# Optimization experiments

Measured on AMD Instinct MI355X. Metric: run time of the kernel, lower is better.

The kernel has to match this reference:

```python
import jax, jax.numpy as jnp
import numpy as np
import math

# Config (matches init_kwargs)
H = 16        # n_heads
DH = 64       # n_dim_head
L = 8         # n_layers
D = 1024      # n_dim
FF = 4096     # n_dim_ffn
NNB = 1       # n_non_bias_tokens
B, T = 2, 1024
EPS = 1e-5


def _slopes(n):
    start = 2.0 ** (-2.0 ** (-(math.log2(n) - 3)))
    return -np.array([start * start ** i for i in range(n)], dtype=np.float32)


def _alibi(seq_len):
    cl = seq_len - NNB
    pos = np.arange(cl)
    rel = np.abs(pos[None, :] - pos[:, None]).astype(np.float32)  # [cl, cl]
    bias = _slopes(H)[:, None, None] * rel                         # [H, cl, cl]
    bias = np.pad(bias, ((0, 0), (0, NNB), (0, NNB)))              # [H, T, T]
    return jnp.asarray(bias)[None]                                  # [1, H, T, T]


def _ln(x, g):
    mu = jnp.mean(x, -1, keepdims=True)
    var = jnp.mean(jnp.square(x - mu), -1, keepdims=True)
    return (x - mu) * jax.lax.rsqrt(var + EPS) * g


def setup_inputs() -> dict:
    key = jax.random.key(0)
    ks = jax.random.split(key, 12)
    std = 0.02
    return {
        "x": jax.random.normal(ks[0], (B, T, D), jnp.float32),
        "attn_w": jax.random.normal(ks[1], (L, 3 * H * DH, D), jnp.float32) * std,
        "attn_out_w": jax.random.normal(ks[2], (L, D, H * DH), jnp.float32) * std,
        "mlp_ln_g": jnp.ones((L, D), jnp.float32),
        "mlp_in_w": jax.random.normal(ks[3], (L, FF, D), jnp.float32) * std,
        "mlp_in_b": jnp.zeros((L, FF), jnp.float32),
        "mlp_out_w": jax.random.normal(ks[4], (L, D, FF), jnp.float32) * std,
        "mlp_out_b": jnp.zeros((L, D), jnp.float32),
        "skip_w": jax.random.normal(ks[5], (L // 2, D, 2 * D), jnp.float32) * std,
        "skip_b": jnp.zeros((L // 2, D), jnp.float32),
        "out_ln_g": jnp.ones((D,), jnp.float32),
    }


def _block(x, alibi, aw, aow, mg, miw, mib, mow, mob):
    b, t, _ = x.shape
    # NOTE: original code computes attention_ln(x) but feeds raw x to the QKV
    # projection (LN output discarded) -- replicated faithfully here.
    qkv = jnp.einsum('btd,ed->bte', x, aw)                 # [B,T,3*H*DH]
    q, k, v = jnp.split(qkv, 3, axis=-1)
    def heads(z):
        return z.reshape(b, t, H, DH).transpose(0, 2, 1, 3)  # [B,H,T,DH]
    q, k, v = heads(q), heads(k), heads(v)
    scores = jnp.einsum('bhqd,bhkd->bhqk', q, k) / math.sqrt(DH) + alibi
    p = jax.nn.softmax(scores, axis=-1)
    o = jnp.einsum('bhqk,bhkd->bhqd', p, v)
    o = o.transpose(0, 2, 1, 3).reshape(b, t, H * DH)
    x = x + jnp.einsum('bte,de->btd', o, aow)
    h = _ln(x, mg)
    h = jax.nn.gelu(jnp.einsum('btd,fd->btf', h, miw) + mib, approximate=False)
    x = x + jnp.einsum('btf,df->btd', h, mow) + mob
    return x


def reference(x, attn_w, attn_out_w, mlp_ln_g, mlp_in_w, mlp_in_b,
              mlp_out_w, mlp_out_b, skip_w, skip_b, out_ln_g):
    _, t, _ = x.shape
    alibi = _alibi(t)
    half = L // 2
    connections = []
    for i in range(L):
        if L - half < i:
            s = connections.pop() * (2.0 ** -0.5)
            xc = jnp.concatenate([x, s], axis=-1)
            j = i - half
            x = jnp.einsum('bte,de->btd', xc, skip_w[j]) + skip_b[j]
        x = _block(x, alibi, attn_w[i], attn_out_w[i], mlp_ln_g[i],
                   mlp_in_w[i], mlp_in_b[i], mlp_out_w[i], mlp_out_b[i])
        if i <= half:
            connections.append(x)
    return _ln(x, out_ln_g)
```

## Files before the change

### kernel.cpp

```cpp
#include <hip/hip_runtime.h>
#include <hip/hip_bf16.h>
#include <math.h>

typedef unsigned short us;
typedef short bf16x8 __attribute__((ext_vector_type(8)));
typedef float f32x4 __attribute__((ext_vector_type(4)));
typedef unsigned short usx4 __attribute__((ext_vector_type(4)));

#define NT   2048
#define DDIM 1024
#define FF   4096
#define TT   1024
#define NH   16
#define CL   1023

__device__ __forceinline__ us f2bf(float f) {
  unsigned u = __float_as_uint(f);
  return (us)((u + 0x7FFFu + ((u >> 16) & 1u)) >> 16);
}

__device__ __forceinline__ void gld_lds16(const us* g, us* l) {
  __builtin_amdgcn_global_load_lds(
      (const __attribute__((address_space(1))) unsigned int*)(g),
      (__attribute__((address_space(3))) unsigned int*)(l), 16, 0, 0);
}

__device__ __forceinline__ void cast_seg(const float* s, us* d, int n4, int tid, int stride) {
  if (n4 <= 0) return;
  for (int i = tid; i < n4; i += stride) {
    float4 v = ((const float4*)s)[i];
    usx4 o; o.x = f2bf(v.x); o.y = f2bf(v.y); o.z = f2bf(v.z); o.w = f2bf(v.w);
    ((usx4*)d)[i] = o;
  }
}

__global__ void cast5_kernel(const float* s0, us* d0, int n0,
                             const float* s1, us* d1, int n1,
                             const float* s2, us* d2, int n2,
                             const float* s3, us* d3, int n3,
                             const float* s4, us* d4, int n4) {
  int tid = blockIdx.x * blockDim.x + threadIdx.x;
  int stride = gridDim.x * blockDim.x;
  cast_seg(s0, d0, n0, tid, stride);
  cast_seg(s1, d1, n1, tid, stride);
  cast_seg(s2, d2, n2, tid, stride);
  cast_seg(s3, d3, n3, tid, stride);
  cast_seg(s4, d4, n4, tid, stride);
}

__global__ void cast1_kernel(const float* s, us* d, int n4) {
  int tid = blockIdx.x * blockDim.x + threadIdx.x;
  int stride = gridDim.x * blockDim.x;
  cast_seg(s, d, n4, tid, stride);
}

template<int SET>
__global__ void bias_rows_kernel(float* __restrict__ x, const float* __restrict__ bias) {
  int i = blockIdx.x * blockDim.x + threadIdx.x;
  float4 b = ((const float4*)bias)[i & 255];
  if (SET) {
    ((float4*)x)[i] = b;
  } else {
    float4 v = ((float4*)x)[i];
    v.x += b.x; v.y += b.y; v.z += b.z; v.w += b.w;
    ((float4*)x)[i] = v;
  }
}

template<int MODE>
__global__ __launch_bounds__(256)
void gemm4(const us* __restrict__ A, const us* __restrict__ W,
           const float* __restrict__ bias, float* outf, us* outb,
           us* __restrict__ Qb, us* __restrict__ Kb, us* __restrict__ Vt,
           int M, int N, int K, int kchunk)
{
  __shared__ us As[64 * 32];
  __shared__ us Ws[128 * 32];
  const int tid = threadIdx.x;
  const int m0 = blockIdx.y * 64, n0 = blockIdx.x * 128;
  const int wave = tid >> 6, lane = tid & 63;
  const int wm = (wave & 1) * 32, wn = (wave >> 1) * 64;
  const int frow = lane & 15, fk = (lane >> 4) * 8;
  const int kbeg = blockIdx.z * kchunk, kend = kbeg + kchunk;
  const int ar = tid >> 2, ac = (tid & 3) * 8;
  const int wr1 = (256 + tid) >> 2;
  f32x4 acc[2][4] = {};
  for (int k0 = kbeg; k0 < kend; k0 += 32) {
    gld_lds16(A + (size_t)(m0 + ar) * K + k0 + ac, As + wave * 512);
    gld_lds16(W + (size_t)(n0 + ar) * K + k0 + ac, Ws + wave * 512);
    gld_lds16(W + (size_t)(n0 + wr1) * K + k0 + ac, Ws + 2048 + wave * 512);
    __syncthreads();
    bf16x8 afr[2], wfr[4];
    #pragma unroll
    for (int i = 0; i < 2; ++i) afr[i] = *(const bf16x8*)(As + (wm + i * 16 + frow) * 32 + fk);
    #pragma unroll
    for (int j = 0; j < 4; ++j) wfr[j] = *(const bf16x8*)(Ws + (wn + j * 16 + frow) * 32 + fk);
    #pragma unroll
    for (int i = 0; i < 2; ++i)
      #pragma unroll
      for (int j = 0; j < 4; ++j)
        acc[i][j] = __builtin_amdgcn_mfma_f32_16x16x32_bf16(afr[i], wfr[j], acc[i][j], 0, 0, 0);
    __syncthreads();
  }
  const int col = lane & 15, rq = (lane >> 4) * 4;
  #pragma unroll
  for (int i = 0; i < 2; ++i) {
    const int gmq = m0 + wm + i * 16 + rq;
    #pragma unroll
    for (int j = 0; j < 4; ++j) {
      const int gn = n0 + wn + j * 16 + col;
      if (MODE == 5) {
        const int t = gmq & (TT - 1), b = gmq >> 10;
        if (gn < DDIM) {
          const int h = gn >> 6, d = gn & 63;
          us* qp = Qb + ((size_t)(b * NH + h) * TT + t) * 64 + d;
          #pragma unroll
          for (int r = 0; r < 4; ++r) qp[(size_t)r * 64] = f2bf(acc[i][j][r] * 0.125f);
        } else if (gn < 2 * DDIM) {
          const int h = (gn - DDIM) >> 6, d = gn & 63;
          us* kp = Kb + ((size_t)(b * NH + h) * TT + t) * 64 + d;
          #pragma unroll
          for (int r = 0; r < 4; ++r) kp[(size_t)r * 64] = f2bf(acc[i][j][r]);
        } else {
          const int h = (gn - 2 * DDIM) >> 6, d = gn & 63;
          usx4 o;
          o.x = f2bf(acc[i][j][0]); o.y = f2bf(acc[i][j][1]);
          o.z = f2bf(acc[i][j][2]); o.w = f2bf(acc[i][j][3]);
          *(usx4*)(Vt + ((size_t)(b * NH + h) * 64 + d) * TT + t) = o;
        }
      } else {
        #pragma unroll
        for (int r = 0; r < 4; ++r) {
          const size_t oi = (size_t)(gmq + r) * N + gn;
          float v = acc[i][j][r];
          if (MODE == 2) {
            float tb = v + bias[gn];
            outb[oi] = f2bf(0.5f * tb * (1.0f + erff(tb * 0.70710678118654752f)));
          }
          if (MODE == 6) atomicAdd(outf + oi, v);
        }
      }
    }
  }
}

__global__ __launch_bounds__(256)
void attn_mfma_kernel(const us* __restrict__ Qb, const us* __restrict__ Kb,
                      const us* __restrict__ Vt, us* __restrict__ obf) {
  __shared__ us Ks[64 * 72];
  __shared__ us Vs[64 * 72];
  __shared__ us Ps[4][16 * 72];
  const int bh = blockIdx.y;
  const int h = bh & (NH - 1), b = bh >> 4;
  const int q0 = blockIdx.x * 64;
  const int tid = threadIdx.x, wave = tid >> 6, lane = tid & 63;
  const float slope = -exp2f(-0.5f * (float)(h + 1));
  const size_t kvbase = (size_t)bh * TT * 64;
  const size_t vtbase = (size_t)bh * 64 * TT;
  const int col = lane & 15, grp = lane >> 4, rq = grp * 4;
  const int qbase = q0 + wave * 16;
  us* Psw = Ps[wave];
  bf16x8 qfrag[2];
  {
    const us* qp = Qb + kvbase + (size_t)(qbase + col) * 64 + grp * 8;
    qfrag[0] = *(const bf16x8*)(qp);
    qfrag[1] = *(const bf16x8*)(qp + 32);
  }
  f32x4 Oacc[4] = {};
  float mrow[4], lrow[4];
  #pragma unroll
  for (int r = 0; r < 4; ++r) { mrow[r] = -3e38f; lrow[r] = 0.0f; }
  for (int kt = 0; kt < 16; ++kt) {
    const int k0 = kt * 64;
    __syncthreads();
    #pragma unroll
    for (int p = 0; p < 2; ++p) {
      int idx = tid * 8 + p * 2048;
      int r = idx >> 6, c = idx & 63;
      *(bf16x8*)(Ks + r * 72 + c) = *(const bf16x8*)(Kb + kvbase + (size_t)(k0 + r) * 64 + c);
      *(bf16x8*)(Vs + r * 72 + c) = *(const bf16x8*)(Vt + vtbase + (size_t)r * TT + k0 + c);
    }
    __syncthreads();
    f32x4 sacc[4];
    #pragma unroll
    for (int ni = 0; ni < 4; ++ni) {
      const us* kp = Ks + (ni * 16 + col) * 72 + grp * 8;
      bf16x8 kf0 = *(const bf16x8*)(kp);
      bf16x8 kf1 = *(const bf16x8*)(kp + 32);
      f32x4 a = {};
      a = __builtin_amdgcn_mfma_f32_16x16x32_bf16(qfrag[0], kf0, a, 0, 0, 0);
      a = __builtin_amdgcn_mfma_f32_16x16x32_bf16(qfrag[1], kf1, a, 0, 0, 0);
      sacc[ni] = a;
    }
    float pmax[4];
    #pragma unroll
    for (int r = 0; r < 4; ++r) pmax[r] = -3e38f;
    #pragma unroll
    for (int ni = 0; ni < 4; ++ni) {
      int kglob = k0 + ni * 16 + col;
      #pragma unroll
      for (int r = 0; r < 4; ++r) {
        int qglob = qbase + rq + r;
        float ab = (qglob < CL && kglob < CL) ? slope * fabsf((float)(kglob - qglob)) : 0.0f;
        sacc[ni][r] += ab;
        pmax[r] = fmaxf(pmax[r], sacc[ni][r]);
      }
    }
    #pragma unroll
    for (int off = 1; off < 16; off <<= 1)
      #pragma unroll
      for (int r = 0; r < 4; ++r)
        pmax[r] = fmaxf(pmax[r], __shfl_xor(pmax[r], off, 64));
    float alpha[4], psum[4];
    #pragma unroll
    for (int r = 0; r < 4; ++r) {
      float mnew = fmaxf(mrow[r], pmax[r]);
      alpha[r] = __expf(mrow[r] - mnew);
      mrow[r] = mnew;
      psum[r] = 0.0f;
    }
    #pragma unroll
    for (int ni = 0; ni < 4; ++ni)
      #pragma unroll
      for (int r = 0; r < 4; ++r) {
        float pv = __expf(sacc[ni][r] - mrow[r]);
        psum[r] += pv;
        Psw[(rq + r) * 72 + ni * 16 + col] = f2bf(pv);
      }
    #pragma unroll
    for (int off = 1; off < 16; off <<= 1)
      #pragma unroll
      for (int r = 0; r < 4; ++r)
        psum[r] += __shfl_xor(psum[r], off, 64);
    #pragma unroll
    for (int r = 0; r < 4; ++r) lrow[r] = alpha[r] * lrow[r] + psum[r];
    #pragma unroll
    for (int ni = 0; ni < 4; ++ni)
      #pragma unroll
      for (int r = 0; r < 4; ++r) Oacc[ni][r] *= alpha[r];
    bf16x8 pf0 = *(const bf16x8*)(Psw + col * 72 + grp * 8);
    bf16x8 pf1 = *(const bf16x8*)(Psw + col * 72 + 32 + grp * 8);
    #pragma unroll
    for (int ni = 0; ni < 4; ++ni) {
      const us* vp = Vs + (ni * 16 + col) * 72 + grp * 8;
      bf16x8 vf0 = *(const bf16x8*)(vp);
      bf16x8 vf1 = *(const bf16x8*)(vp + 32);
      Oacc[ni] = __builtin_amdgcn_mfma_f32_16x16x32_bf16(pf0, vf0, Oacc[ni], 0, 0, 0);
      Oacc[ni] = __builtin_amdgcn_mfma_f32_16x16x32_bf16(pf1, vf1, Oacc[ni], 0, 0, 0);
    }
  }
  #pragma unroll
  for (int ni = 0; ni < 4; ++ni)
    #pragma unroll
    for (int r = 0; r < 4; ++r) {
      size_t token = (size_t)b * TT + qbase + rq + r;
      obf[token * DDIM + h * 64 + ni * 16 + col] = f2bf(Oacc[ni][r] / lrow[r]);
    }
}

template<int BF16OUT>
__global__ __launch_bounds__(256)
void ln_kernel(const float* __restrict__ x, const float* __restrict__ g,
               float* outf, us* outb) {
  __shared__ float red[256];
  const int rowi = blockIdx.x, t = threadIdx.x;
  const float* xr = x + (size_t)rowi * DDIM;
  float4 v = ((const float4*)xr)[t];
  red[t] = v.x + v.y + v.z + v.w;
  __syncthreads();
  for (int off = 128; off > 0; off >>= 1) {
    if (t < off) red[t] += red[t + off];
    __syncthreads();
  }
  float mu = red[0] * (1.0f / 1024.0f);
  __syncthreads();
  float dx = v.x - mu, dy = v.y - mu, dz = v.z - mu, dw = v.w - mu;
  red[t] = dx * dx + dy * dy + dz * dz + dw * dw;
  __syncthreads();
  for (int off = 128; off > 0; off >>= 1) {
    if (t < off) red[t] += red[t + off];
    __syncthreads();
  }
  float rs = rsqrtf(red[0] * (1.0f / 1024.0f) + 1e-5f);
  float4 gg = ((const float4*)g)[t];
  if (BF16OUT) {
    usx4 o;
    o.x = f2bf(dx * rs * gg.x); o.y = f2bf(dy * rs * gg.y);
    o.z = f2bf(dz * rs * gg.z); o.w = f2bf(dw * rs * gg.w);
    ((usx4*)(outb + (size_t)rowi * DDIM))[t] = o;
  } else {
    float4 o;
    o.x = dx * rs * gg.x; o.y = dy * rs * gg.y; o.z = dz * rs * gg.z; o.w = dw * rs * gg.w;
    ((float4*)(outf + (size_t)rowi * DDIM))[t] = o;
  }
}

__global__ void concat_cast_kernel(const float* __restrict__ x, const float* __restrict__ s,
                                   us* __restrict__ out) {
  int i4 = blockIdx.x * blockDim.x + threadIdx.x;
  int e = i4 * 4;
  int r = e >> 11, c = e & 2047;
  float4 v;
  if (c < DDIM) {
    v = *(const float4*)(x + (size_t)r * DDIM + c);
  } else {
    v = *(const float4*)(s + (size_t)r * DDIM + (c - DDIM));
    v.x *= 0.70710678118654752f; v.y *= 0.70710678118654752f;
    v.z *= 0.70710678118654752f; v.w *= 0.70710678118654752f;
  }
  usx4 o; o.x = f2bf(v.x); o.y = f2bf(v.y); o.z = f2bf(v.z); o.w = f2bf(v.w);
  ((usx4*)out)[i4] = o;
}

extern "C" void kernel_launch(void* const* d_in, const int* in_sizes, int n_in,
                              void* d_out, int out_size, void* d_ws, size_t ws_size,
                              hipStream_t stream) {
  (void)in_sizes; (void)n_in; (void)out_size; (void)ws_size;
  const float* x_in       = (const float*)d_in[0];
  const float* attn_w     = (const float*)d_in[1];
  const float* attn_out_w = (const float*)d_in[2];
  const float* mlp_ln_g   = (const float*)d_in[3];
  const float* mlp_in_w   = (const float*)d_in[4];
  const float* mlp_in_b   = (const float*)d_in[5];
  const float* mlp_out_w  = (const float*)d_in[6];
  const float* mlp_out_b  = (const float*)d_in[7];
  const float* skip_w     = (const float*)d_in[8];
  const float* skip_b     = (const float*)d_in[9];
  const float* out_ln_g   = (const float*)d_in[10];

  char* p = (char*)d_ws;
  auto alloc = [&](size_t bytes) { char* r = p; p += (bytes + 255) & ~(size_t)255; return r; };
  float* xbuf = (float*)alloc((size_t)NT * DDIM * 4);
  float* conn = (float*)alloc((size_t)3 * NT * DDIM * 4);
  us* Qb   = (us*)alloc((size_t)NT * DDIM * 2);
  us* Kb   = (us*)alloc((size_t)NT * DDIM * 2);
  us* Vt   = (us*)alloc((size_t)NT * DDIM * 2);
  us* xbf  = (us*)alloc((size_t)NT * DDIM * 2);
  us* obf  = (us*)alloc((size_t)NT * DDIM * 2);
  us* hln  = (us*)alloc((size_t)NT * DDIM * 2);
  us* hbf  = (us*)alloc((size_t)NT * FF * 2);
  us* xcbf = (us*)alloc((size_t)NT * 2 * DDIM * 2);
  us* wqkv = (us*)alloc((size_t)3 * DDIM * DDIM * 2);
  us* wao  = (us*)alloc((size_t)DDIM * DDIM * 2);
  us* wmi  = (us*)alloc((size_t)FF * DDIM * 2);
  us* wmo  = (us*)alloc((size_t)DDIM * FF * 2);
  us* wsk  = (us*)alloc((size_t)DDIM * 2 * DDIM * 2);

  hipMemcpyAsync(xbuf, x_in, (size_t)NT * DDIM * 4, hipMemcpyDeviceToDevice, stream);

  for (int i = 0; i < 8; ++i) {
    const int do_skip = (i >= 5);
    cast5_kernel<<<1024, 256, 0, stream>>>(
        attn_w + (size_t)i * 3 * DDIM * DDIM, wqkv, 3 * DDIM * DDIM / 4,
        attn_out_w + (size_t)i * DDIM * DDIM, wao, DDIM * DDIM / 4,
        mlp_in_w + (size_t)i * FF * DDIM, wmi, FF * DDIM / 4,
        mlp_out_w + (size_t)i * DDIM * FF, wmo, DDIM * FF / 4,
        do_skip ? (skip_w + (size_t)(i - 4) * DDIM * 2 * DDIM) : nullptr, wsk,
        do_skip ? (DDIM * 2 * DDIM / 4) : 0);
    if (do_skip) {
      concat_cast_kernel<<<4096, 256, 0, stream>>>(xbuf, conn + (size_t)(7 - i) * NT * DDIM, xcbf);
      bias_rows_kernel<1><<<NT, 256, 0, stream>>>(xbuf, skip_b + (size_t)(i - 4) * DDIM);
      gemm4<6><<<dim3(8, 32, 2), 256, 0, stream>>>(
          xcbf, wsk, nullptr, xbuf, nullptr, nullptr, nullptr, nullptr,
          NT, DDIM, 2 * DDIM, DDIM);
    }
    cast1_kernel<<<1024, 256, 0, stream>>>(xbuf, xbf, NT * DDIM / 4);
    gemm4<5><<<dim3(24, 32, 1), 256, 0, stream>>>(
        xbf, wqkv, nullptr, nullptr, nullptr, Qb, Kb, Vt,
        NT, 3 * DDIM, DDIM, DDIM);
    attn_mfma_kernel<<<dim3(TT / 64, 2 * NH), 256, 0, stream>>>(Qb, Kb, Vt, obf);
    gemm4<6><<<dim3(8, 32, 2), 256, 0, stream>>>(
        obf, wao, nullptr, xbuf, nullptr, nullptr, nullptr, nullptr,
        NT, DDIM, DDIM, DDIM / 2);
    ln_kernel<1><<<NT, 256, 0, stream>>>(xbuf, mlp_ln_g + (size_t)i * DDIM, nullptr, hln);
    gemm4<2><<<dim3(32, 32, 1), 256, 0, stream>>>(
        hln, wmi, mlp_in_b + (size_t)i * FF, nullptr, hbf, nullptr, nullptr, nullptr,
        NT, FF, DDIM, DDIM);
    bias_rows_kernel<0><<<NT, 256, 0, stream>>>(xbuf, mlp_out_b + (size_t)i * DDIM);
    gemm4<6><<<dim3(8, 32, 4), 256, 0, stream>>>(
        hbf, wmo, nullptr, xbuf, nullptr, nullptr, nullptr, nullptr,
        NT, DDIM, FF, DDIM);
    if (i >= 2 && i <= 4)
      hipMemcpyAsync(conn + (size_t)(i - 2) * NT * DDIM, xbuf, (size_t)NT * DDIM * 4,
                     hipMemcpyDeviceToDevice, stream);
  }
  ln_kernel<0><<<NT, 256, 0, stream>>>(xbuf, out_ln_g, (float*)d_out, nullptr);
}
```

Before: 2.033 ms.

## Replace split-K atomic GEMMs with BN=64 tiles and fused bias/residual epilogues

Result: faster. 1.919 ms (-5.6%).

```diff
diff --git a/kernel.cpp b/kernel.cpp
--- a/kernel.cpp
+++ b/kernel.cpp
@@ -54,20 +54,7 @@
   cast_seg(s, d, n4, tid, stride);
 }
 
-template<int SET>
-__global__ void bias_rows_kernel(float* __restrict__ x, const float* __restrict__ bias) {
-  int i = blockIdx.x * blockDim.x + threadIdx.x;
-  float4 b = ((const float4*)bias)[i & 255];
-  if (SET) {
-    ((float4*)x)[i] = b;
-  } else {
-    float4 v = ((float4*)x)[i];
-    v.x += b.x; v.y += b.y; v.z += b.z; v.w += b.w;
-    ((float4*)x)[i] = v;
-  }
-}
-
-template<int MODE>
+template<int MODE, int BN>
 __global__ __launch_bounds__(256)
 void gemm4(const us* __restrict__ A, const us* __restrict__ W,
            const float* __restrict__ bias, float* outf, us* outb,
@@ -75,30 +62,32 @@
            int M, int N, int K, int kchunk)
 {
   __shared__ us As[64 * 32];
-  __shared__ us Ws[128 * 32];
+  __shared__ us Ws[BN * 32];
   const int tid = threadIdx.x;
-  const int m0 = blockIdx.y * 64, n0 = blockIdx.x * 128;
+  const int m0 = blockIdx.y * 64, n0 = blockIdx.x * BN;
   const int wave = tid >> 6, lane = tid & 63;
-  const int wm = (wave & 1) * 32, wn = (wave >> 1) * 64;
+  const int wm = (wave & 1) * 32, wn = (wave >> 1) * (BN >> 1);
   const int frow = lane & 15, fk = (lane >> 4) * 8;
   const int kbeg = blockIdx.z * kchunk, kend = kbeg + kchunk;
   const int ar = tid >> 2, ac = (tid & 3) * 8;
   const int wr1 = (256 + tid) >> 2;
-  f32x4 acc[2][4] = {};
+  constexpr int NJ = BN / 32;
+  f32x4 acc[2][NJ] = {};
   for (int k0 = kbeg; k0 < kend; k0 += 32) {
     gld_lds16(A + (size_t)(m0 + ar) * K + k0 + ac, As + wave * 512);
     gld_lds16(W + (size_t)(n0 + ar) * K + k0 + ac, Ws + wave * 512);
-    gld_lds16(W + (size_t)(n0 + wr1) * K + k0 + ac, Ws + 2048 + wave * 512);
-    __syncthreads();
-    bf16x8 afr[2], wfr[4];
+    if (BN == 128)
+      gld_lds16(W + (size_t)(n0 + wr1) * K + k0 + ac, Ws + 2048 + wave * 512);
+    __syncthreads();
+    bf16x8 afr[2], wfr[NJ];
     #pragma unroll
     for (int i = 0; i < 2; ++i) afr[i] = *(const bf16x8*)(As + (wm + i * 16 + frow) * 32 + fk);
     #pragma unroll
-    for (int j = 0; j < 4; ++j) wfr[j] = *(const bf16x8*)(Ws + (wn + j * 16 + frow) * 32 + fk);
+    for (int j = 0; j < NJ; ++j) wfr[j] = *(const bf16x8*)(Ws + (wn + j * 16 + frow) * 32 + fk);
     #pragma unroll
     for (int i = 0; i < 2; ++i)
       #pragma unroll
-      for (int j = 0; j < 4; ++j)
+      for (int j = 0; j < NJ; ++j)
         acc[i][j] = __builtin_amdgcn_mfma_f32_16x16x32_bf16(afr[i], wfr[j], acc[i][j], 0, 0, 0);
     __syncthreads();
   }
@@ -107,7 +96,7 @@
   for (int i = 0; i < 2; ++i) {
     const int gmq = m0 + wm + i * 16 + rq;
     #pragma unroll
-    for (int j = 0; j < 4; ++j) {
+    for (int j = 0; j < NJ; ++j) {
       const int gn = n0 + wn + j * 16 + col;
       if (MODE == 5) {
         const int t = gmq & (TT - 1), b = gmq >> 10;
@@ -137,7 +126,17 @@
             float tb = v + bias[gn];
             outb[oi] = f2bf(0.5f * tb * (1.0f + erff(tb * 0.70710678118654752f)));
           }
-          if (MODE == 6) atomicAdd(outf + oi, v);
+          if (MODE == 7) {
+            outf[oi] = v + outf[oi];
+          }
+          if (MODE == 8) {
+            float w = v + bias[gn] + outf[oi];
+            outf[oi] = w; outb[oi] = f2bf(w);
+          }
+          if (MODE == 9) {
+            float w = v + bias[gn];
+            outf[oi] = w; outb[oi] = f2bf(w);
+          }
         }
       }
     }
@@ -347,6 +346,7 @@
   us* wsk  = (us*)alloc((size_t)DDIM * 2 * DDIM * 2);
 
   hipMemcpyAsync(xbuf, x_in, (size_t)NT * DDIM * 4, hipMemcpyDeviceToDevice, stream);
+  cast1_kernel<<<1024, 256, 0, stream>>>(x_in, xbf, NT * DDIM / 4);
 
   for (int i = 0; i < 8; ++i) {
     const int do_skip = (i >= 5);
@@ -359,27 +359,24 @@
         do_skip ? (DDIM * 2 * DDIM / 4) : 0);
     if (do_skip) {
       concat_cast_kernel<<<4096, 256, 0, stream>>>(xbuf, conn + (size_t)(7 - i) * NT * DDIM, xcbf);
-      bias_rows_kernel<1><<<NT, 256, 0, stream>>>(xbuf, skip_b + (size_t)(i - 4) * DDIM);
-      gemm4<6><<<dim3(8, 32, 2), 256, 0, stream>>>(
-          xcbf, wsk, nullptr, xbuf, nullptr, nullptr, nullptr, nullptr,
-          NT, DDIM, 2 * DDIM, DDIM);
-    }
-    cast1_kernel<<<1024, 256, 0, stream>>>(xbuf, xbf, NT * DDIM / 4);
-    gemm4<5><<<dim3(24, 32, 1), 256, 0, stream>>>(
+      gemm4<9, 64><<<dim3(16, 32, 1), 256, 0, stream>>>(
+          xcbf, wsk, skip_b + (size_t)(i - 4) * DDIM, xbuf, xbf, nullptr, nullptr, nullptr,
+          NT, DDIM, 2 * DDIM, 2 * DDIM);
+    }
+    gemm4<5, 128><<<dim3(24, 32, 1), 256, 0, stream>>>(
         xbf, wqkv, nullptr, nullptr, nullptr, Qb, Kb, Vt,
         NT, 3 * DDIM, DDIM, DDIM);
     attn_mfma_kernel<<<dim3(TT / 64, 2 * NH), 256, 0, stream>>>(Qb, Kb, Vt, obf);
-    gemm4<6><<<dim3(8, 32, 2), 256, 0, stream>>>(
+    gemm4<7, 64><<<dim3(16, 32, 1), 256, 0, stream>>>(
         obf, wao, nullptr, xbuf, nullptr, nullptr, nullptr, nullptr,
-        NT, DDIM, DDIM, DDIM / 2);
+        NT, DDIM, DDIM, DDIM);
     ln_kernel<1><<<NT, 256, 0, stream>>>(xbuf, mlp_ln_g + (size_t)i * DDIM, nullptr, hln);
-    gemm4<2><<<dim3(32, 32, 1), 256, 0, stream>>>(
+    gemm4<2, 128><<<dim3(32, 32, 1), 256, 0, stream>>>(
         hln, wmi, mlp_in_b + (size_t)i * FF, nullptr, hbf, nullptr, nullptr, nullptr,
         NT, FF, DDIM, DDIM);
-    bias_rows_kernel<0><<<NT, 256, 0, stream>>>(xbuf, mlp_out_b + (size_t)i * DDIM);
-    gemm4<6><<<dim3(8, 32, 4), 256, 0, stream>>>(
-        hbf, wmo, nullptr, xbuf, nullptr, nullptr, nullptr, nullptr,
-        NT, DDIM, FF, DDIM);
+    gemm4<8, 64><<<dim3(16, 32, 1), 256, 0, stream>>>(
+        hbf, wmo, mlp_out_b + (size_t)i * DDIM, xbuf, xbf, nullptr, nullptr, nullptr,
+        NT, DDIM, FF, FF);
     if (i >= 2 && i <= 4)
       hipMemcpyAsync(conn + (size_t)(i - 2) * NT * DDIM, xbuf, (size_t)NT * DDIM * 4,
                      hipMemcpyDeviceToDevice, stream);
```
